# Performance work log

Measured on AMD Instinct MI355X. Metric: run time of the kernel, lower is better.

## Reference

```python
import jax, jax.numpy as jnp
import numpy as np

IN_BIT = 8
W_BIT = 8
B, CIN, COUT = 4096, 2048, 2048


def _uq(x, k):
    # uniform_quantize forward math (k-bit fake quantization)
    n = float(2 ** k - 1)
    return jnp.round(x * n) / n


def setup_inputs() -> dict:
    key = jax.random.key(0)
    k1, k2 = jax.random.split(key)
    x = jax.random.uniform(k1, (B, CIN), dtype=jnp.float32)  # inputs in [0,1] (clamped by quantizer)
    # kaiming-normal-like init for weight [COUT, CIN]
    weight = jax.random.normal(k2, (COUT, CIN), dtype=jnp.float32) * np.float32((2.0 / CIN) ** 0.5)
    # default (unassigned) phases: first half -pi/2, second half +pi/2
    half = CIN // 2
    phases = jnp.concatenate(
        [jnp.full((1, 1, half), -np.pi / 2, dtype=jnp.float32),
         jnp.full((1, 1, CIN - half), np.pi / 2, dtype=jnp.float32)], axis=2)
    disks = jnp.ones((1, 1, CIN, 2), dtype=jnp.float32)
    return {"x": x, "weight": weight, "phases": phases, "disks": disks}


def reference(x, weight, phases, disks):
    # --- input quantization: uniform_q(clamp(x,0,1)) ---
    xq = _uq(jnp.clip(x, 0.0, 1.0), IN_BIT)                      # [B, CIN]
    # --- weight quantization (dorefa): tanh, normalize to [0,1], quantize ---
    w = jnp.tanh(weight)
    w = w / (2.0 * jnp.max(jnp.abs(w))) + 0.5
    wq = _uq(w, W_BIT)                                            # [COUT, CIN]
    # --- optical (homodyne) linear with phase/disk modulation ---
    # out = 0.25 * sum_i (I+ - I-)
    # With ideal phases (sin = +/-1) and unit disks this reduces to x @ (w * sign).T
    sin_phi = jnp.sin(phases)[0, 0]                               # [CIN]
    d0 = disks[0, 0, :, 0]
    d1 = disks[0, 0, :, 1]
    dd = d0 - d1                                                  # [CIN]
    ds = d0 + d1                                                  # [CIN]
    term_x = (xq * xq) @ dd                                       # [B]
    term_w = (wq * wq) @ dd                                       # [COUT]
    cross = jnp.einsum('bi,oi->bo', xq, wq * (sin_phi * ds))      # [B, COUT]
    out = 0.25 * (term_x[:, None] + term_w[None, :] + 2.0 * cross)
    return out
```

## Files before the change

kernel.cpp:

```cpp
#include <hip/hip_runtime.h>
#include <hip/hip_bf16.h>
#include <math.h>

#define B_DIM 4096
#define CIN   2048
#define COUT  2048

typedef float f32x4  __attribute__((ext_vector_type(4)));
typedef int   i32x4  __attribute__((ext_vector_type(4)));
typedef int   i32x16 __attribute__((ext_vector_type(16)));
typedef char  c8x8   __attribute__((ext_vector_type(8)));

__device__ inline float wave_reduce_sum(float v) {
#pragma unroll
    for (int off = 32; off > 0; off >>= 1)
        v += __shfl_down(v, off, 64);
    return v;
}
__device__ inline float wave_reduce_max(float v) {
#pragma unroll
    for (int off = 32; off > 0; off >>= 1)
        v = fmaxf(v, __shfl_down(v, off, 64));
    return v;
}

#define NMAXBLK 256
__global__ void prep_a_kernel(const float* __restrict__ x,
                              const float* __restrict__ weight,
                              const float* __restrict__ phases,
                              const float* __restrict__ disks,
                              char* __restrict__ XQ8,
                              float* __restrict__ term_x,
                              float* __restrict__ pmax,
                              float* __restrict__ s_tab,
                              float* __restrict__ dd_tab,
                              float* __restrict__ smax_buf) {
    __shared__ float red[4];
    const int blk = blockIdx.x;
    const int tid = threadIdx.x;

    if (blk < B_DIM) {
        const float* xr = x + (size_t)blk * CIN + tid * 8;
        const f32x4* dk = (const f32x4*)(disks + (size_t)tid * 16);
        f32x4 v0 = ((const f32x4*)xr)[0];
        f32x4 v1 = ((const f32x4*)xr)[1];
        c8x8 h;
        float sum = 0.f;
#pragma unroll
        for (int j = 0; j < 8; ++j) {
            float xv = (j < 4) ? v0[j] : v1[j - 4];
            float qr = rintf(fminf(fmaxf(xv, 0.f), 1.f) * 255.f);
            float q  = qr * (1.f / 255.f);
            f32x4 dv = dk[j >> 1];
            float d0 = dv[(j & 1) * 2], d1 = dv[(j & 1) * 2 + 1];
            sum += q * q * (d0 - d1);
            h[j] = (char)(int)(qr - 128.f);
        }
        *(c8x8*)(XQ8 + (size_t)blk * CIN + tid * 8) = h;
        sum = wave_reduce_sum(sum);
        if ((tid & 63) == 0) red[tid >> 6] = sum;
        __syncthreads();
        if (tid == 0)
            term_x[blk] = 0.25f * (red[0] + red[1] + red[2] + red[3]);
    } else if (blk < B_DIM + NMAXBLK) {
        const int mb = blk - B_DIM;
        const size_t n4 = (size_t)COUT * CIN / 4;
        const f32x4* w4 = (const f32x4*)weight;
        float m = 0.f;
        for (size_t i = (size_t)mb * 256 + tid; i < n4; i += (size_t)NMAXBLK * 256) {
            f32x4 v = w4[i];
            m = fmaxf(m, fmaxf(fmaxf(fabsf(v[0]), fabsf(v[1])),
                               fmaxf(fabsf(v[2]), fabsf(v[3]))));
        }
        m = wave_reduce_max(m);
        if ((tid & 63) == 0) red[tid >> 6] = m;
        __syncthreads();
        if (tid == 0)
            pmax[mb] = fmaxf(fmaxf(red[0], red[1]), fmaxf(red[2], red[3]));
    } else {
        float lmax = 0.f;
        for (int i = tid; i < CIN; i += 256) {
            float d0 = disks[2 * i], d1 = disks[2 * i + 1];
            float s  = sinf(phases[i]) * (d0 + d1);
            s_tab[i]  = s;
            dd_tab[i] = d0 - d1;
            lmax = fmaxf(lmax, fabsf(s));
        }
        lmax = wave_reduce_max(lmax);
        if ((tid & 63) == 0) red[tid >> 6] = lmax;
        __syncthreads();
        if (tid == 0)
            smax_buf[0] = fmaxf(fmaxf(fmaxf(red[0], red[1]),
                                      fmaxf(red[2], red[3])), 1e-20f);
    }
}

__global__ void prep_b_kernel(const float* __restrict__ weight,
                              const float* __restrict__ pmax,
                              const float* __restrict__ s_tab,
                              const float* __restrict__ dd_tab,
                              const float* __restrict__ smax_buf,
                              char* __restrict__ V8,
                              float* __restrict__ term_w2) {
    __shared__ float red[4];
    __shared__ float bmax;
    const int tid = threadIdx.x;

    float m = pmax[tid];
    m = wave_reduce_max(m);
    if ((tid & 63) == 0) red[tid >> 6] = m;
    __syncthreads();
    if (tid == 0)
        bmax = tanhf(fmaxf(fmaxf(red[0], red[1]), fmaxf(red[2], red[3])));
    __syncthreads();
    const float inv2m = 0.5f / bmax;
    const float smax  = smax_buf[0];
    const float k127  = 127.f / smax;

    const int o = blockIdx.x;
    const float* wr  = weight + (size_t)o * CIN + tid * 8;
    const f32x4* w4  = (const f32x4*)wr;
    const f32x4* s4  = (const f32x4*)(s_tab  + tid * 8);
    const f32x4* dd4 = (const f32x4*)(dd_tab + tid * 8);
    float sumdd = 0.f, sb = 0.f;
    c8x8 h;
#pragma unroll
    for (int half = 0; half < 2; ++half) {
        f32x4 wv = w4[half], sv = s4[half], ddv = dd4[half];
#pragma unroll
        for (int j = 0; j < 4; ++j) {
            float t  = tanhf(wv[j]);
            float wq = rintf((t * inv2m + 0.5f) * 255.f) * (1.f / 255.f);
            sumdd += wq * wq * ddv[j];
            float bp = rintf(wq * sv[j] * k127);
            sb += bp;
            h[half * 4 + j] = (char)(int)bp;
        }
    }
    *(c8x8*)(V8 + (size_t)o * CIN + tid * 8) = h;

    sumdd = wave_reduce_sum(sumdd);
    sb    = wave_reduce_sum(sb);
    if ((tid & 63) == 0) red[tid >> 6] = sumdd;
    __syncthreads();
    float sumdd_t = red[0] + red[1] + red[2] + red[3];
    __syncthreads();
    if ((tid & 63) == 0) red[tid >> 6] = sb;
    __syncthreads();
    if (tid == 0) {
        float sb_t = red[0] + red[1] + red[2] + red[3];
        term_w2[o] = 0.25f * sumdd_t + (64.f * smax / 32385.f) * sb_t;
    }
}

#define BM 256
#define BN 128
#define BKB 128
#define NT (CIN / BKB)

#define MEMFENCE asm volatile("" ::: "memory")
#define BARRIER() do { MEMFENCE; __builtin_amdgcn_s_barrier(); MEMFENCE; } while (0)
#define VMCNT(N) asm volatile("s_waitcnt vmcnt(" #N ")" ::: "memory")

__global__ __launch_bounds__(512, 2) void
gemm_kernel(const char* __restrict__ A,
            const char* __restrict__ Bw,
            const float* __restrict__ term_x,
            const float* __restrict__ term_w2,
            const float* __restrict__ smax_buf,
            float* __restrict__ C) {
    __shared__ __align__(16) char As[3][BM * BKB];
    __shared__ __align__(16) char Bs[3][BN * BKB];

    const int tid  = threadIdx.x;
    const int wave = tid >> 6;
    const int lane = tid & 63;

    const int wg  = blockIdx.x;
    const int xcd = wg & 7;
    const int idx = wg >> 3;
    const int tile_m = (xcd >> 1) * 4 + (idx >> 3);
    const int tile_n = (xcd & 1) * 8 + (idx & 7);
    const int row0 = tile_m * BM;
    const int col0 = tile_n * BN;
    const int wr = wave >> 1;
    const int wc = wave & 1;

    i32x16 acc[2][2];
#pragma unroll
    for (int m = 0; m < 2; ++m)
#pragma unroll
        for (int n = 0; n < 2; ++n)
#pragma unroll
            for (int j = 0; j < 16; ++j)
                acc[m][n][j] = 0;

    const int st_row = lane >> 3;
    const int st_g   = lane & 7;
    const char* Agp = A  + (size_t)row0 * CIN;
    const char* Bgp = Bw + (size_t)col0 * CIN;

    const int rl = lane & 31;
    const int hi = lane >> 5;
    const int fxor = (rl & 7) ^ (((rl >> 4) & 1) << 1);

    int offA[4][2], offB[4][2];
#pragma unroll
    for (int ks = 0; ks < 4; ++ks)
#pragma unroll
        for (int m = 0; m < 2; ++m) {
            const int pg = ((ks * 2 + hi) ^ fxor) * 16;
            offA[ks][m] = (wr * 64 + m * 32 + rl) * BKB + pg;
            offB[ks][m] = (wc * 64 + m * 32 + rl) * BKB + pg;
        }

#define STAGE(buf, k0) do {                                                    \
    _Pragma("unroll")                                                          \
    for (int j = 0; j < 4; ++j) {                 \
        const int chunk = wave + j * 8;                                        \
        const int rr = chunk * 8 + st_row;                                     \
        const int sc = (st_g ^ st_row ^ (((chunk >> 1) & 1) << 1)) * 16;       \
        __builtin_amdgcn_global_load_lds(                                      \
            (const __attribute__((address_space(1))) void*)(Agp + (size_t)rr * CIN + (k0) + sc), \
            (__attribute__((address_space(3))) void*)(&As[buf][chunk * 1024]), \
            16, 0, 0);                                                         \
    }                                                                          \
    _Pragma("unroll")                                                          \
    for (int j = 0; j < 2; ++j) {                 \
        const int chunk = wave + j * 8;                                        \
        const int rr = chunk * 8 + st_row;                                     \
        const int sc = (st_g ^ st_row ^ (((chunk >> 1) & 1) << 1)) * 16;       \
        __builtin_amdgcn_global_load_lds(                                      \
            (const __attribute__((address_space(1))) void*)(Bgp + (size_t)rr * CIN + (k0) + sc), \
            (__attribute__((address_space(3))) void*)(&Bs[buf][chunk * 1024]), \
            16, 0, 0);                                                         \
    } } while (0)

#define TILE(bufc, STAGE_STMT, VM_STMT) do {                                   \
    STAGE_STMT;                                                                \
    _Pragma("unroll")                                                          \
    for (int ks = 0; ks < 4; ++ks) {                                           \
        i32x4 a0 = *(const i32x4*)(&As[bufc][offA[ks][0]]);                    \
        i32x4 a1 = *(const i32x4*)(&As[bufc][offA[ks][1]]);                    \
        i32x4 b0 = *(const i32x4*)(&Bs[bufc][offB[ks][0]]);                    \
        i32x4 b1 = *(const i32x4*)(&Bs[bufc][offB[ks][1]]);                    \
        __builtin_amdgcn_s_setprio(1);                                         \
        acc[0][0] = __builtin_amdgcn_mfma_i32_32x32x32_i8(a0, b0, acc[0][0], 0, 0, 0); \
        acc[0][1] = __builtin_amdgcn_mfma_i32_32x32x32_i8(a0, b1, acc[0][1], 0, 0, 0); \
        acc[1][0] = __builtin_amdgcn_mfma_i32_32x32x32_i8(a1, b0, acc[1][0], 0, 0, 0); \
        acc[1][1] = __builtin_amdgcn_mfma_i32_32x32x32_i8(a1, b1, acc[1][1], 0, 0, 0); \
        __builtin_amdgcn_s_setprio(0);                                         \
    }                                                                          \
    VM_STMT;                                                                   \
    BARRIER();                                                                 \
} while (0)

    STAGE(0, 0);
    STAGE(1, BKB);
    VMCNT(6);
    BARRIER();

    int k0 = 0;
#pragma unroll 1
    for (int grp = 0; grp < 4; ++grp) {
        TILE(0, STAGE(2, k0 + 2 * BKB), VMCNT(6));
        TILE(1, STAGE(0, k0 + 3 * BKB), VMCNT(6));
        TILE(2, STAGE(1, k0 + 4 * BKB), VMCNT(6));
        k0 += 3 * BKB;
    }
    TILE(0, STAGE(2, 14 * BKB), VMCNT(6));
    TILE(1, STAGE(0, 15 * BKB), VMCNT(6));
    TILE(2, (void)0, VMCNT(0));
    TILE(0, (void)0, (void)0);

    const float coef = 0.5f * smax_buf[0] / 32385.f;
#pragma unroll
    for (int m = 0; m < 2; ++m)
#pragma unroll
        for (int n = 0; n < 2; ++n) {
            const int c = col0 + wc * 64 + n * 32 + rl;
            const float tw = term_w2[c];
#pragma unroll
            for (int reg = 0; reg < 16; ++reg) {
                const int r = row0 + wr * 64 + m * 32 +
                              (reg & 3) + 8 * (reg >> 2) + 4 * hi;
                C[(size_t)r * COUT + c] =
                    coef * (float)acc[m][n][reg] + term_x[r] + tw;
            }
        }
#undef STAGE
#undef TILE
}

extern "C" void kernel_launch(void* const* d_in, const int* in_sizes, int n_in,
                              void* d_out, int out_size, void* d_ws, size_t ws_size,
                              hipStream_t stream) {
    const float* x      = (const float*)d_in[0];
    const float* weight = (const float*)d_in[1];
    const float* phases = (const float*)d_in[2];
    const float* disks  = (const float*)d_in[3];
    float* out = (float*)d_out;

    char* ws = (char*)d_ws;
    float* pmax     = (float*)(ws);
    float* smax_buf = (float*)(ws + 1024);
    float* s_tab    = (float*)(ws + 4096);
    float* dd_tab   = (float*)(ws + 16384);
    float* term_w2  = (float*)(ws + 32768);
    float* term_x   = (float*)(ws + 49152);
    char* XQ8 = (char*)(ws + 65536);
    char* V8  = (char*)(ws + 65536 + (size_t)B_DIM * CIN);

    prep_a_kernel<<<B_DIM + NMAXBLK + 1, 256, 0, stream>>>(
        x, weight, phases, disks, XQ8, term_x, pmax, s_tab, dd_tab, smax_buf);
    prep_b_kernel<<<COUT, 256, 0, stream>>>(
        weight, pmax, s_tab, dd_tab, smax_buf, V8, term_w2);
    gemm_kernel<<<(B_DIM / BM) * (COUT / BN), 512, 0, stream>>>(
        XQ8, V8, term_x, term_w2, smax_buf, out);
}
```

Before: 47.94 us.

## Shrink GEMM tile to 128x128 with 4 waves and double-buffered LDS

The int8 GEMM tile shrinks from 256x128 with 8 waves to 128x128 with 4 waves, doubling the workgroup count to 512. The triple-buffered LDS pipeline with partial vmcnt waits becomes a simpler double buffer that waits for all loads before each barrier. The XCD-aware tile mapping is updated to cover the extra M tiles. This raises occupancy and grid size but lowers data reuse per tile, and the full vmcnt(0) waits reduce overlap between loads and MFMA work.

```diff
diff --git a/kernel.cpp b/kernel.cpp
--- a/kernel.cpp
+++ b/kernel.cpp
@@ -153,24 +153,24 @@
     }
 }
 
-#define BM 256
+#define BM 128
 #define BN 128
 #define BKB 128
 #define NT (CIN / BKB)
 
 #define MEMFENCE asm volatile("" ::: "memory")
 #define BARRIER() do { MEMFENCE; __builtin_amdgcn_s_barrier(); MEMFENCE; } while (0)
-#define VMCNT(N) asm volatile("s_waitcnt vmcnt(" #N ")" ::: "memory")
-
-__global__ __launch_bounds__(512, 2) void
+#define VMCNT0 asm volatile("s_waitcnt vmcnt(0)" ::: "memory")
+
+__global__ __launch_bounds__(256, 2) void
 gemm_kernel(const char* __restrict__ A,
             const char* __restrict__ Bw,
             const float* __restrict__ term_x,
             const float* __restrict__ term_w2,
             const float* __restrict__ smax_buf,
             float* __restrict__ C) {
-    __shared__ __align__(16) char As[3][BM * BKB];
-    __shared__ __align__(16) char Bs[3][BN * BKB];
+    __shared__ __align__(16) char As[2][BM * BKB];
+    __shared__ __align__(16) char Bs[2][BN * BKB];
 
     const int tid  = threadIdx.x;
     const int wave = tid >> 6;
@@ -179,7 +179,7 @@
     const int wg  = blockIdx.x;
     const int xcd = wg & 7;
     const int idx = wg >> 3;
-    const int tile_m = (xcd >> 1) * 4 + (idx >> 3);
+    const int tile_m = (xcd >> 1) * 8 + (idx >> 3);
     const int tile_n = (xcd & 1) * 8 + (idx & 7);
     const int row0 = tile_m * BM;
     const int col0 = tile_n * BN;
@@ -216,62 +216,49 @@
 
 #define STAGE(buf, k0) do {                                                    \
     _Pragma("unroll")                                                          \
-    for (int j = 0; j < 4; ++j) {                 \
-        const int chunk = wave + j * 8;                                        \
+    for (int j = 0; j < 4; ++j) {           \
+        const int chunk = wave + j * 4;                                        \
         const int rr = chunk * 8 + st_row;                                     \
         const int sc = (st_g ^ st_row ^ (((chunk >> 1) & 1) << 1)) * 16;       \
         __builtin_amdgcn_global_load_lds(                                      \
             (const __attribute__((address_space(1))) void*)(Agp + (size_t)rr * CIN + (k0) + sc), \
             (__attribute__((address_space(3))) void*)(&As[buf][chunk * 1024]), \
             16, 0, 0);                                                         \
-    }                                                                          \
-    _Pragma("unroll")                                                          \
-    for (int j = 0; j < 2; ++j) {                 \
-        const int chunk = wave + j * 8;                                        \
-        const int rr = chunk * 8 + st_row;                                     \
-        const int sc = (st_g ^ st_row ^ (((chunk >> 1) & 1) << 1)) * 16;       \
         __builtin_amdgcn_global_load_lds(                                      \
             (const __attribute__((address_space(1))) void*)(Bgp + (size_t)rr * CIN + (k0) + sc), \
             (__attribute__((address_space(3))) void*)(&Bs[buf][chunk * 1024]), \
             16, 0, 0);                                                         \
     } } while (0)
 
-#define TILE(bufc, STAGE_STMT, VM_STMT) do {                                   \
-    STAGE_STMT;                                                                \
+#define COMPUTE(buf) do {                                                      \
     _Pragma("unroll")                                                          \
     for (int ks = 0; ks < 4; ++ks) {                                           \
-        i32x4 a0 = *(const i32x4*)(&As[bufc][offA[ks][0]]);                    \
-        i32x4 a1 = *(const i32x4*)(&As[bufc][offA[ks][1]]);                    \
-        i32x4 b0 = *(const i32x4*)(&Bs[bufc][offB[ks][0]]);                    \
-        i32x4 b1 = *(const i32x4*)(&Bs[bufc][offB[ks][1]]);                    \
+        i32x4 a0 = *(const i32x4*)(&As[buf][offA[ks][0]]);                     \
+        i32x4 a1 = *(const i32x4*)(&As[buf][offA[ks][1]]);                     \
+        i32x4 b0 = *(const i32x4*)(&Bs[buf][offB[ks][0]]);                     \
+        i32x4 b1 = *(const i32x4*)(&Bs[buf][offB[ks][1]]);                     \
         __builtin_amdgcn_s_setprio(1);                                         \
         acc[0][0] = __builtin_amdgcn_mfma_i32_32x32x32_i8(a0, b0, acc[0][0], 0, 0, 0); \
         acc[0][1] = __builtin_amdgcn_mfma_i32_32x32x32_i8(a0, b1, acc[0][1], 0, 0, 0); \
         acc[1][0] = __builtin_amdgcn_mfma_i32_32x32x32_i8(a1, b0, acc[1][0], 0, 0, 0); \
         acc[1][1] = __builtin_amdgcn_mfma_i32_32x32x32_i8(a1, b1, acc[1][1], 0, 0, 0); \
         __builtin_amdgcn_s_setprio(0);                                         \
-    }                                                                          \
-    VM_STMT;                                                                   \
-    BARRIER();                                                                 \
-} while (0)
+    } } while (0)
 
     STAGE(0, 0);
-    STAGE(1, BKB);
-    VMCNT(6);
+    VMCNT0;
     BARRIER();
 
-    int k0 = 0;
 #pragma unroll 1
-    for (int grp = 0; grp < 4; ++grp) {
-        TILE(0, STAGE(2, k0 + 2 * BKB), VMCNT(6));
-        TILE(1, STAGE(0, k0 + 3 * BKB), VMCNT(6));
-        TILE(2, STAGE(1, k0 + 4 * BKB), VMCNT(6));
-        k0 += 3 * BKB;
+    for (int t = 0; t < NT; t += 2) {
+        STAGE(1, (t + 1) * BKB);
+        COMPUTE(0);
+        VMCNT0;
+        BARRIER();
+        if (t + 2 < NT) STAGE(0, (t + 2) * BKB);
+        COMPUTE(1);
+        if (t + 2 < NT) { VMCNT0; BARRIER(); }
     }
-    TILE(0, STAGE(2, 14 * BKB), VMCNT(6));
-    TILE(1, STAGE(0, 15 * BKB), VMCNT(6));
-    TILE(2, (void)0, VMCNT(0));
-    TILE(0, (void)0, (void)0);
 
     const float coef = 0.5f * smax_buf[0] / 32385.f;
 #pragma unroll
@@ -289,7 +276,7 @@
             }
         }
 #undef STAGE
-#undef TILE
+#undef COMPUTE
 }
 
 extern "C" void kernel_launch(void* const* d_in, const int* in_sizes, int n_in,
@@ -315,6 +302,6 @@
         x, weight, phases, disks, XQ8, term_x, pmax, s_tab, dd_tab, smax_buf);
     prep_b_kernel<<<COUT, 256, 0, stream>>>(
         weight, pmax, s_tab, dd_tab, smax_buf, V8, term_w2);
-    gemm_kernel<<<(B_DIM / BM) * (COUT / BN), 512, 0, stream>>>(
+    gemm_kernel<<<(B_DIM / BM) * (COUT / BN), 256, 0, stream>>>(
         XQ8, V8, term_x, term_w2, smax_buf, out);
 }
```

Measured after the change: 48.78 us. Within noise of the previous version (+1.7%).
